# Kernel tuning notes

Hardware: AMD Instinct MI355X
Metric: run time of the kernel (lower is better)

Reference implementation:

```python
import jax, jax.numpy as jnp
import numpy as np

N = 100000
E = 2000000
F = 64          # in_features == out_features (required by attention * h_j)
BETA = 0.5
NEG_SLOPE = 0.01  # torch F.leaky_relu default


def setup_inputs() -> dict:
    key = jax.random.key(0)
    k1, k2, k3, k4, k5, k6 = jax.random.split(key, 6)
    h = jax.random.normal(k1, (N, F), dtype=jnp.float32)
    adj = jax.random.randint(k2, (2, E), 0, N, dtype=jnp.int64)
    amount = jax.random.uniform(k3, (E,), dtype=jnp.float32)
    count = jax.random.uniform(k4, (E,), dtype=jnp.float32)
    fc_w = jax.random.normal(k5, (F, 2 * F), dtype=jnp.float32) * (1.0 / np.sqrt(2 * F))
    fc_b = jax.random.normal(k6, (F,), dtype=jnp.float32) * 0.01
    return {"h": h, "adj": adj, "amount": amount, "count": count,
            "fc_w": fc_w, "fc_b": fc_b}


def _minmax_norm(x):
    lo, hi = x.min(), x.max()
    return (x - lo) / (hi - lo + 1e-8)


def reference(h, adj, amount, count, fc_w, fc_b):
    # per-edge weight from normalized amount/count
    edge_weight = BETA * _minmax_norm(amount) + (1.0 - BETA) * _minmax_norm(count)  # [E]

    src, dst = adj[0], adj[1]
    h_i = h[src]                     # [E, F]
    h_j = h[dst]                     # [E, F]
    h_cat = jnp.concatenate([h_i, h_j], axis=1)  # [E, 2F]

    score = jnp.einsum('ef,of->eo', h_cat, fc_w) + fc_b  # [E, F_out]
    score = jnp.where(score >= 0, score, NEG_SLOPE * score)  # leaky_relu
    score = score * edge_weight[:, None]

    # softmax over ALL edges (dim 0), per feature, as in the original
    attention = jax.nn.softmax(score, axis=0)  # [E, F]

    agg = jnp.zeros_like(h).at[src].add(attention * h_j)  # scatter-add -> [N, F]
    return agg
```

## Files before the change

kernel.cpp:

```cpp
#include <hip/hip_runtime.h>
#include <hip/hip_fp16.h>
#include <math.h>

#define FDIM   64
#define NB     16
#define MMB    512
#define BSHIFT 7
#define BMASK  127
#define EPTA   16
#define CHUNKA (EPTA * 256)
#define SCH    1024
#define DMASK  0xFFFFF

__global__ __launch_bounds__(256) void minmax1_k(const float* __restrict__ amount,
                                                 const float* __restrict__ count,
                                                 float4* __restrict__ partial,
                                                 double* __restrict__ colsum, int E4) {
  int idx = blockIdx.x * blockDim.x + threadIdx.x;
  int stride = gridDim.x * blockDim.x;
  if (idx < 64) colsum[idx] = 0.0;
  float amin = 3.4e38f, amax = -3.4e38f, cmin = 3.4e38f, cmax = -3.4e38f;
  const float4* a4 = (const float4*)amount;
  const float4* c4 = (const float4*)count;
  for (int i = idx; i < E4; i += stride) {
    float4 a = a4[i], c = c4[i];
    amin = fminf(amin, fminf(fminf(a.x, a.y), fminf(a.z, a.w)));
    amax = fmaxf(amax, fmaxf(fmaxf(a.x, a.y), fmaxf(a.z, a.w)));
    cmin = fminf(cmin, fminf(fminf(c.x, c.y), fminf(c.z, c.w)));
    cmax = fmaxf(cmax, fmaxf(fmaxf(c.x, c.y), fmaxf(c.z, c.w)));
  }
  #pragma unroll
  for (int off = 32; off; off >>= 1) {
    amin = fminf(amin, __shfl_down(amin, off));
    amax = fmaxf(amax, __shfl_down(amax, off));
    cmin = fminf(cmin, __shfl_down(cmin, off));
    cmax = fmaxf(cmax, __shfl_down(cmax, off));
  }
  __shared__ float4 lds[4];
  if ((threadIdx.x & 63) == 0) lds[threadIdx.x >> 6] = make_float4(amin, amax, cmin, cmax);
  __syncthreads();
  if (threadIdx.x == 0) {
    float4 r = lds[0];
    #pragma unroll
    for (int w = 1; w < 4; w++) {
      r.x = fminf(r.x, lds[w].x); r.y = fmaxf(r.y, lds[w].y);
      r.z = fminf(r.z, lds[w].z); r.w = fmaxf(r.w, lds[w].w);
    }
    partial[blockIdx.x] = r;
  }
}

__global__ __launch_bounds__(256) void minmax2_k(const float4* __restrict__ partial,
                                                 const float* __restrict__ amount,
                                                 const float* __restrict__ count,
                                                 float* __restrict__ mmf,
                                                 int nb, int E4, int E) {
  float amin = 3.4e38f, amax = -3.4e38f, cmin = 3.4e38f, cmax = -3.4e38f;
  for (int i = threadIdx.x; i < nb; i += 256) {
    float4 p = partial[i];
    amin = fminf(amin, p.x); amax = fmaxf(amax, p.y);
    cmin = fminf(cmin, p.z); cmax = fmaxf(cmax, p.w);
  }
  for (int i = 4 * E4 + threadIdx.x; i < E; i += 256) {
    float a = amount[i], c = count[i];
    amin = fminf(amin, a); amax = fmaxf(amax, a);
    cmin = fminf(cmin, c); cmax = fmaxf(cmax, c);
  }
  #pragma unroll
  for (int off = 32; off; off >>= 1) {
    amin = fminf(amin, __shfl_down(amin, off));
    amax = fmaxf(amax, __shfl_down(amax, off));
    cmin = fminf(cmin, __shfl_down(cmin, off));
    cmax = fmaxf(cmax, __shfl_down(cmax, off));
  }
  __shared__ float4 lds[4];
  if ((threadIdx.x & 63) == 0) lds[threadIdx.x >> 6] = make_float4(amin, amax, cmin, cmax);
  __syncthreads();
  if (threadIdx.x == 0) {
    float4 r = lds[0];
    #pragma unroll
    for (int w = 1; w < 4; w++) {
      r.x = fminf(r.x, lds[w].x); r.y = fmaxf(r.y, lds[w].y);
      r.z = fminf(r.z, lds[w].z); r.w = fmaxf(r.w, lds[w].w);
    }
    mmf[0] = r.x; mmf[1] = r.y; mmf[2] = r.z; mmf[3] = r.w;
  }
}

__global__ __launch_bounds__(256) void binA_count_k(const int* __restrict__ src,
                                                    int* __restrict__ mat,
                                                    int E, int nblkA, int nbkt) {
  __shared__ int lhist[1024];
  for (int k = threadIdx.x; k < nbkt; k += 256) lhist[k] = 0;
  __syncthreads();
  int e0 = blockIdx.x * CHUNKA + threadIdx.x * EPTA;
  if (e0 + EPTA <= E) {
    #pragma unroll
    for (int q = 0; q < EPTA; q += 4) {
      int4 s4 = *(const int4*)(src + e0 + q);
      atomicAdd(&lhist[s4.x >> BSHIFT], 1);
      atomicAdd(&lhist[s4.y >> BSHIFT], 1);
      atomicAdd(&lhist[s4.z >> BSHIFT], 1);
      atomicAdd(&lhist[s4.w >> BSHIFT], 1);
    }
  } else {
    for (int e = e0; e < E; e++) atomicAdd(&lhist[src[e] >> BSHIFT], 1);
  }
  __syncthreads();
  for (int k = threadIdx.x; k < nbkt; k += 256)
    mat[(size_t)k * nblkA + blockIdx.x] = lhist[k];
}

__global__ __launch_bounds__(256) void scan1_k(const int* __restrict__ v,
                                               int* __restrict__ bsum, int M) {
  __shared__ int lds[256];
  int t = threadIdx.x, b = blockIdx.x;
  int s = 0;
  for (int i = b * SCH + t; i < min((b + 1) * SCH, M); i += 256) s += v[i];
  lds[t] = s; __syncthreads();
  for (int off = 128; off; off >>= 1) {
    if (t < off) lds[t] += lds[t + off];
    __syncthreads();
  }
  if (t == 0) bsum[b] = lds[0];
}

__global__ __launch_bounds__(256) void scan2_k(const int* __restrict__ bsum,
                                               int* __restrict__ bexcl, int nchunk) {
  __shared__ int lds[256];
  int t = threadIdx.x;
  int running = 0;
  for (int c0 = 0; c0 < nchunk; c0 += 256) {
    int x = (c0 + t < nchunk) ? bsum[c0 + t] : 0;
    lds[t] = x; __syncthreads();
    for (int off = 1; off < 256; off <<= 1) {
      int v = (t >= off) ? lds[t - off] : 0;
      __syncthreads();
      lds[t] += v; __syncthreads();
    }
    if (c0 + t < nchunk) bexcl[c0 + t] = running + lds[t] - x;
    running += lds[255];
    __syncthreads();
  }
}

__global__ __launch_bounds__(256) void scan3_k(const int* __restrict__ v,
                                               const int* __restrict__ bexcl,
                                               int* __restrict__ smat, int M) {
  __shared__ int lds[256];
  int t = threadIdx.x, b = blockIdx.x;
  int running = bexcl[b];
  for (int tile = 0; tile < SCH; tile += 256) {
    int i = b * SCH + tile + t;
    int x = (i < M) ? v[i] : 0;
    lds[t] = x; __syncthreads();
    for (int off = 1; off < 256; off <<= 1) {
      int vv = (t >= off) ? lds[t - off] : 0;
      __syncthreads();
      lds[t] += vv; __syncthreads();
    }
    if (i < M) smat[i] = running + lds[t] - x;
    running += lds[255];
    __syncthreads();
  }
}

__global__ __launch_bounds__(256) void binA_scatter_k(const int* __restrict__ src,
                                                      const int* __restrict__ dst,
                                                      const float* __restrict__ amount,
                                                      const float* __restrict__ count,
                                                      const float* __restrict__ mmf,
                                                      const int* __restrict__ smat,
                                                      int2* __restrict__ payload,
                                                      int E, int nblkA, int nbkt) {
  __shared__ int lcur[1024];
  for (int k = threadIdx.x; k < nbkt; k += 256)
    lcur[k] = smat[(size_t)k * nblkA + blockIdx.x];
  __syncthreads();
  const float amin = mmf[0], amax = mmf[1], cmin = mmf[2], cmax = mmf[3];
  const float ascale = 0.5f / (amax - amin + 1e-8f);
  const float cscale = 0.5f / (cmax - cmin + 1e-8f);
  int e0 = blockIdx.x * CHUNKA + threadIdx.x * EPTA;
  if (e0 + EPTA <= E) {
    #pragma unroll
    for (int q = 0; q < EPTA; q += 4) {
      int4   s4 = *(const int4*)(src + e0 + q);
      int4   d4 = *(const int4*)(dst + e0 + q);
      float4 a4 = *(const float4*)(amount + e0 + q);
      float4 c4 = *(const float4*)(count + e0 + q);
      float w0 = (a4.x - amin) * ascale + (c4.x - cmin) * cscale;
      float w1 = (a4.y - amin) * ascale + (c4.y - cmin) * cscale;
      float w2 = (a4.z - amin) * ascale + (c4.z - cmin) * cscale;
      float w3 = (a4.w - amin) * ascale + (c4.w - cmin) * cscale;
      int p0 = atomicAdd(&lcur[s4.x >> BSHIFT], 1);
      int p1 = atomicAdd(&lcur[s4.y >> BSHIFT], 1);
      int p2 = atomicAdd(&lcur[s4.z >> BSHIFT], 1);
      int p3 = atomicAdd(&lcur[s4.w >> BSHIFT], 1);
      payload[p0] = make_int2(d4.x | ((s4.x & BMASK) << 20), __float_as_int(w0));
      payload[p1] = make_int2(d4.y | ((s4.y & BMASK) << 20), __float_as_int(w1));
      payload[p2] = make_int2(d4.z | ((s4.z & BMASK) << 20), __float_as_int(w2));
      payload[p3] = make_int2(d4.w | ((s4.w & BMASK) << 20), __float_as_int(w3));
    }
  } else {
    for (int e = e0; e < E; e++) {
      int s = src[e];
      float ew = (amount[e] - amin) * ascale + (count[e] - cmin) * cscale;
      int pos = atomicAdd(&lcur[s >> BSHIFT], 1);
      payload[pos] = make_int2(dst[e] | ((s & BMASK) << 20), __float_as_int(ew));
    }
  }
}

__global__ __launch_bounds__(256) void binB_k(const int2* __restrict__ payload,
                                              const int* __restrict__ smat,
                                              int* __restrict__ hist,
                                              int* __restrict__ offsets,
                                              int2* __restrict__ edge_s,
                                              int E, int nblkA, int nbkt, int N) {
  __shared__ int fcnt[128];
  __shared__ int fs[128];
  __shared__ int fcur[128];
  const int b = blockIdx.x;
  const int t = threadIdx.x;
  const int base = smat[(size_t)b * nblkA];
  const int end  = (b + 1 < nbkt) ? smat[(size_t)(b + 1) * nblkA] : E;
  if (t < 128) fcnt[t] = 0;
  __syncthreads();
  for (int i = base + t; i < end; i += 256)
    atomicAdd(&fcnt[payload[i].x >> 20], 1);
  __syncthreads();
  if (t < 128) fs[t] = fcnt[t];
  __syncthreads();
  for (int off = 1; off < 128; off <<= 1) {
    int v = 0;
    if (t < 128 && t >= off) v = fs[t - off];
    __syncthreads();
    if (t < 128) fs[t] += v;
    __syncthreads();
  }
  if (t < 128) {
    int excl = fs[t] - fcnt[t];
    fcur[t] = base + excl;
    int node = (b << BSHIFT) + t;
    if (node < N) { hist[node] = fcnt[t]; offsets[node] = base + excl; }
  }
  __syncthreads();
  for (int i = base + t; i < end; i += 256) {
    int2 v = payload[i];
    int pos = atomicAdd(&fcur[v.x >> 20], 1);
    edge_s[pos] = make_int2(v.x & DMASK, v.y);
  }
}

__global__ __launch_bounds__(128) void pre_gemm(const float* __restrict__ h,
                                                const float* __restrict__ fc_w,
                                                const float* __restrict__ fc_b,
                                                float* __restrict__ G1,
                                                __half2* __restrict__ P, int N) {
  __shared__ float hs[NB * FDIM];
  const int t = threadIdx.x;
  const int o = t & 63, half = t >> 6;
  float w[FDIM];
  const float* wrow = fc_w + o * 128 + half * 64;
  #pragma unroll
  for (int f = 0; f < FDIM; f += 4) {
    float4 v = *(const float4*)(wrow + f);
    w[f] = v.x; w[f + 1] = v.y; w[f + 2] = v.z; w[f + 3] = v.w;
  }
  const float bias = (half == 0) ? fc_b[o] : 0.0f;
  const int n0 = blockIdx.x * NB;
  const int nrows = min(NB, N - n0);
  for (int i = t; i < nrows * FDIM; i += 128) hs[i] = h[(size_t)n0 * FDIM + i];
  __syncthreads();
  for (int n = 0; n < nrows; n++) {
    float acc = bias;
    #pragma unroll
    for (int f = 0; f < FDIM; f += 4) {
      float4 hv = *(const float4*)(&hs[n * FDIM + f]);
      acc += hv.x * w[f] + hv.y * w[f + 1] + hv.z * w[f + 2] + hv.w * w[f + 3];
    }
    if (half == 0) {
      G1[(size_t)(n0 + n) * FDIM + o] = acc;
    } else {
      P[(size_t)(n0 + n) * FDIM + o] =
          __halves2half2(__float2half(acc), __float2half(hs[n * FDIM + o]));
    }
  }
}

__device__ __forceinline__ float2 unpack_h2(unsigned u) {
  __half2 v = *(__half2*)&u;
  return make_float2(__low2float(v), __high2float(v));
}

__global__ __launch_bounds__(256) void fused_k(const int* __restrict__ offsets,
                                               const int* __restrict__ hist,
                                               const int2* __restrict__ edge_s,
                                               const float* __restrict__ G1,
                                               const unsigned* __restrict__ P,
                                               double* __restrict__ colsum,
                                               float* __restrict__ out, int N) {
  const int lane = threadIdx.x & 63;
  const int wid = blockIdx.x * 4 + (threadIdx.x >> 6);
  const int nw = gridDim.x * 4;
  float csum = 0.0f;
  for (int n = wid; n < N; n += nw) {
    float g1 = G1[(size_t)n * FDIM + lane];
    float acc = 0.0f;
    int start = offsets[n], cnt = hist[n];
    for (int j0 = 0; j0 < cnt; j0 += 64) {
      int m = min(64, cnt - j0);
      int2 p = make_int2(0, 0);
      if (lane < m) p = edge_s[start + j0 + lane];
      int j = 0;
      for (; j + 8 <= m; j += 8) {
        int d0 = __builtin_amdgcn_readlane(p.x, j);
        int d1 = __builtin_amdgcn_readlane(p.x, j + 1);
        int d2 = __builtin_amdgcn_readlane(p.x, j + 2);
        int d3 = __builtin_amdgcn_readlane(p.x, j + 3);
        int d4 = __builtin_amdgcn_readlane(p.x, j + 4);
        int d5 = __builtin_amdgcn_readlane(p.x, j + 5);
        int d6 = __builtin_amdgcn_readlane(p.x, j + 6);
        int d7 = __builtin_amdgcn_readlane(p.x, j + 7);
        float e0 = __int_as_float(__builtin_amdgcn_readlane(p.y, j));
        float e1 = __int_as_float(__builtin_amdgcn_readlane(p.y, j + 1));
        float e2 = __int_as_float(__builtin_amdgcn_readlane(p.y, j + 2));
        float e3 = __int_as_float(__builtin_amdgcn_readlane(p.y, j + 3));
        float e4 = __int_as_float(__builtin_amdgcn_readlane(p.y, j + 4));
        float e5 = __int_as_float(__builtin_amdgcn_readlane(p.y, j + 5));
        float e6 = __int_as_float(__builtin_amdgcn_readlane(p.y, j + 6));
        float e7 = __int_as_float(__builtin_amdgcn_readlane(p.y, j + 7));
        unsigned u0 = P[(size_t)d0 * FDIM + lane];
        unsigned u1 = P[(size_t)d1 * FDIM + lane];
        unsigned u2 = P[(size_t)d2 * FDIM + lane];
        unsigned u3 = P[(size_t)d3 * FDIM + lane];
        unsigned u4 = P[(size_t)d4 * FDIM + lane];
        unsigned u5 = P[(size_t)d5 * FDIM + lane];
        unsigned u6 = P[(size_t)d6 * FDIM + lane];
        unsigned u7 = P[(size_t)d7 * FDIM + lane];
        float2 v0 = unpack_h2(u0), v1 = unpack_h2(u1), v2 = unpack_h2(u2), v3 = unpack_h2(u3);
        float2 v4 = unpack_h2(u4), v5 = unpack_h2(u5), v6 = unpack_h2(u6), v7 = unpack_h2(u7);
        float s0 = g1 + v0.x, s1 = g1 + v1.x, s2 = g1 + v2.x, s3 = g1 + v3.x;
        float s4 = g1 + v4.x, s5 = g1 + v5.x, s6 = g1 + v6.x, s7 = g1 + v7.x;
        s0 = (s0 >= 0.0f) ? s0 : 0.01f * s0;  s1 = (s1 >= 0.0f) ? s1 : 0.01f * s1;
        s2 = (s2 >= 0.0f) ? s2 : 0.01f * s2;  s3 = (s3 >= 0.0f) ? s3 : 0.01f * s3;
        s4 = (s4 >= 0.0f) ? s4 : 0.01f * s4;  s5 = (s5 >= 0.0f) ? s5 : 0.01f * s5;
        s6 = (s6 >= 0.0f) ? s6 : 0.01f * s6;  s7 = (s7 >= 0.0f) ? s7 : 0.01f * s7;
        float x0 = __expf(s0 * e0), x1 = __expf(s1 * e1);
        float x2 = __expf(s2 * e2), x3 = __expf(s3 * e3);
        float x4 = __expf(s4 * e4), x5 = __expf(s5 * e5);
        float x6 = __expf(s6 * e6), x7 = __expf(s7 * e7);
        csum += ((x0 + x1) + (x2 + x3)) + ((x4 + x5) + (x6 + x7));
        acc += x0 * v0.y + x1 * v1.y + x2 * v2.y + x3 * v3.y;
        acc += x4 * v4.y + x5 * v5.y + x6 * v6.y + x7 * v7.y;
      }
      for (; j < m; j++) {
        int d = __builtin_amdgcn_readlane(p.x, j);
        float ew = __int_as_float(__builtin_amdgcn_readlane(p.y, j));
        float2 v = unpack_h2(P[(size_t)d * FDIM + lane]);
        float sc = g1 + v.x;
        sc = (sc >= 0.0f) ? sc : 0.01f * sc;
        float x = __expf(sc * ew);
        csum += x;
        acc += x * v.y;
      }
    }
    out[(size_t)n * FDIM + lane] = acc;
  }
  __shared__ float part[256];
  part[threadIdx.x] = csum;
  __syncthreads();
  if (threadIdx.x < 64) {
    float tot = part[threadIdx.x] + part[threadIdx.x + 64] +
                part[threadIdx.x + 128] + part[threadIdx.x + 192];
    atomicAdd(&colsum[threadIdx.x], (double)tot);
  }
}

__global__ __launch_bounds__(256) void scale_k(float* __restrict__ out,
                                               const double* __restrict__ colsum,
                                               size_t total) {
  __shared__ float rinv_s[64];
  if (threadIdx.x < 64) rinv_s[threadIdx.x] = (float)(1.0 / colsum[threadIdx.x]);
  __syncthreads();
  const float r = rinv_s[threadIdx.x & 63];
  size_t idx = (size_t)blockIdx.x * blockDim.x + threadIdx.x;
  size_t stride = (size_t)gridDim.x * blockDim.x;
  for (size_t i = idx; i < total; i += stride) out[i] *= r;
}

extern "C" void kernel_launch(void* const* d_in, const int* in_sizes, int n_in,
                              void* d_out, int out_size, void* d_ws, size_t ws_size,
                              hipStream_t stream) {
  const float* h      = (const float*)d_in[0];
  const int*   adj    = (const int*)d_in[1];
  const float* amount = (const float*)d_in[2];
  const float* count  = (const float*)d_in[3];
  const float* fc_w   = (const float*)d_in[4];
  const float* fc_b   = (const float*)d_in[5];
  float* out = (float*)d_out;

  const int E = in_sizes[2];
  const int N = in_sizes[0] / FDIM;
  const int E4 = E / 4;
  const int* src = adj;
  const int* dst = adj + E;
  const int nbkt  = (N + BMASK) >> BSHIFT;
  const int nblkA = (E + CHUNKA - 1) / CHUNKA;
  const int M = nbkt * nblkA;
  const int nchunk = (M + SCH - 1) / SCH;

  char* ws = (char*)d_ws;
  size_t off = 0;
  auto alloc = [&](size_t bytes) { void* p = ws + off; off += (bytes + 255) & ~(size_t)255; return p; };
  float*    G1      = (float*)alloc((size_t)N * FDIM * sizeof(float));
  __half2*  P       = (__half2*)alloc((size_t)N * FDIM * sizeof(__half2));
  int2*     edge_s  = (int2*)alloc((size_t)E * sizeof(int2));
  int2*     payload = (int2*)alloc((size_t)E * sizeof(int2));
  int*      hist    = (int*)alloc((size_t)N * sizeof(int));
  int*      offsets = (int*)alloc((size_t)N * sizeof(int));
  int*      mat     = (int*)alloc((size_t)M * sizeof(int));
  int*      smat    = (int*)alloc((size_t)M * sizeof(int));
  int*      bsum    = (int*)alloc((size_t)nchunk * sizeof(int));
  int*      bexcl   = (int*)alloc((size_t)nchunk * sizeof(int));
  float4*   mmpart  = (float4*)alloc((size_t)MMB * sizeof(float4));
  double*   colsum  = (double*)alloc(64 * sizeof(double));
  float*    mmf     = (float*)alloc(4 * sizeof(float));

  minmax1_k<<<MMB, 256, 0, stream>>>(amount, count, mmpart, colsum, E4);
  minmax2_k<<<1, 256, 0, stream>>>(mmpart, amount, count, mmf, MMB, E4, E);
  binA_count_k<<<nblkA, 256, 0, stream>>>(src, mat, E, nblkA, nbkt);
  scan1_k<<<nchunk, 256, 0, stream>>>(mat, bsum, M);
  scan2_k<<<1, 256, 0, stream>>>(bsum, bexcl, nchunk);
  scan3_k<<<nchunk, 256, 0, stream>>>(mat, bexcl, smat, M);
  binA_scatter_k<<<nblkA, 256, 0, stream>>>(src, dst, amount, count, mmf, smat, payload, E, nblkA, nbkt);
  binB_k<<<nbkt, 256, 0, stream>>>(payload, smat, hist, offsets, edge_s, E, nblkA, nbkt, N);
  pre_gemm<<<(N + NB - 1) / NB, 128, 0, stream>>>(h, fc_w, fc_b, G1, P, N);
  fused_k<<<4096, 256, 0, stream>>>(offsets, hist, edge_s, G1, (const unsigned*)P, colsum, out, N);
  scale_k<<<2048, 256, 0, stream>>>(out, colsum, (size_t)N * FDIM);
}
```

Before: 338.2 us.

## Fuse minmax with bin counting, stage scatter in LDS, prefetch next node

Merges the amount/count min-max reduction into the bucket-count pass, so those arrays are read once and one launch disappears. The bucket scatter now sorts each block's edges locally in LDS before writing them to global memory, which makes the payload writes more contiguous. The aggregation loop prefetches the next node's offsets, G1 row and first edge batch, and replaces the remainder loop with masked groups of 8. The scale kernel is vectorised to float4. These add LDS pressure (about 50KB per scatter block, which may lower occupancy) and some extra wasted work in the masked tails.

Result: faster. 325.6 us (-3.7%).

```diff
diff --git a/kernel.cpp b/kernel.cpp
--- a/kernel.cpp
+++ b/kernel.cpp
@@ -4,7 +4,6 @@
 
 #define FDIM   64
 #define NB     16
-#define MMB    512
 #define BSHIFT 7
 #define BMASK  127
 #define EPTA   16
@@ -12,22 +11,42 @@
 #define SCH    1024
 #define DMASK  0xFFFFF
 
-__global__ __launch_bounds__(256) void minmax1_k(const float* __restrict__ amount,
-                                                 const float* __restrict__ count,
-                                                 float4* __restrict__ partial,
-                                                 double* __restrict__ colsum, int E4) {
-  int idx = blockIdx.x * blockDim.x + threadIdx.x;
-  int stride = gridDim.x * blockDim.x;
-  if (idx < 64) colsum[idx] = 0.0;
+__global__ __launch_bounds__(256) void count_mm_k(const int* __restrict__ src,
+                                                  const float* __restrict__ amount,
+                                                  const float* __restrict__ count,
+                                                  int* __restrict__ mat,
+                                                  float4* __restrict__ partial,
+                                                  double* __restrict__ colsum,
+                                                  int E, int nblkA, int nbkt) {
+  __shared__ int lhist[1024];
+  __shared__ float4 lred[4];
+  for (int k = threadIdx.x; k < nbkt; k += 256) lhist[k] = 0;
+  if (blockIdx.x == 0 && threadIdx.x < 64) colsum[threadIdx.x] = 0.0;
+  __syncthreads();
   float amin = 3.4e38f, amax = -3.4e38f, cmin = 3.4e38f, cmax = -3.4e38f;
-  const float4* a4 = (const float4*)amount;
-  const float4* c4 = (const float4*)count;
-  for (int i = idx; i < E4; i += stride) {
-    float4 a = a4[i], c = c4[i];
-    amin = fminf(amin, fminf(fminf(a.x, a.y), fminf(a.z, a.w)));
-    amax = fmaxf(amax, fmaxf(fmaxf(a.x, a.y), fmaxf(a.z, a.w)));
-    cmin = fminf(cmin, fminf(fminf(c.x, c.y), fminf(c.z, c.w)));
-    cmax = fmaxf(cmax, fmaxf(fmaxf(c.x, c.y), fmaxf(c.z, c.w)));
+  int e0 = blockIdx.x * CHUNKA + threadIdx.x * EPTA;
+  if (e0 + EPTA <= E) {
+    #pragma unroll
+    for (int q = 0; q < EPTA; q += 4) {
+      int4   s4 = *(const int4*)(src + e0 + q);
+      float4 a4 = *(const float4*)(amount + e0 + q);
+      float4 c4 = *(const float4*)(count + e0 + q);
+      atomicAdd(&lhist[s4.x >> BSHIFT], 1);
+      atomicAdd(&lhist[s4.y >> BSHIFT], 1);
+      atomicAdd(&lhist[s4.z >> BSHIFT], 1);
+      atomicAdd(&lhist[s4.w >> BSHIFT], 1);
+      amin = fminf(amin, fminf(fminf(a4.x, a4.y), fminf(a4.z, a4.w)));
+      amax = fmaxf(amax, fmaxf(fmaxf(a4.x, a4.y), fmaxf(a4.z, a4.w)));
+      cmin = fminf(cmin, fminf(fminf(c4.x, c4.y), fminf(c4.z, c4.w)));
+      cmax = fmaxf(cmax, fmaxf(fmaxf(c4.x, c4.y), fmaxf(c4.z, c4.w)));
+    }
+  } else {
+    for (int e = e0; e < E; e++) {
+      atomicAdd(&lhist[src[e] >> BSHIFT], 1);
+      float a = amount[e], c = count[e];
+      amin = fminf(amin, a); amax = fmaxf(amax, a);
+      cmin = fminf(cmin, c); cmax = fmaxf(cmax, c);
+    }
   }
   #pragma unroll
   for (int off = 32; off; off >>= 1) {
@@ -36,35 +55,28 @@
     cmin = fminf(cmin, __shfl_down(cmin, off));
     cmax = fmaxf(cmax, __shfl_down(cmax, off));
   }
-  __shared__ float4 lds[4];
-  if ((threadIdx.x & 63) == 0) lds[threadIdx.x >> 6] = make_float4(amin, amax, cmin, cmax);
-  __syncthreads();
+  if ((threadIdx.x & 63) == 0) lred[threadIdx.x >> 6] = make_float4(amin, amax, cmin, cmax);
+  __syncthreads();
+  for (int k = threadIdx.x; k < nbkt; k += 256)
+    mat[(size_t)k * nblkA + blockIdx.x] = lhist[k];
   if (threadIdx.x == 0) {
-    float4 r = lds[0];
+    float4 r = lred[0];
     #pragma unroll
     for (int w = 1; w < 4; w++) {
-      r.x = fminf(r.x, lds[w].x); r.y = fmaxf(r.y, lds[w].y);
-      r.z = fminf(r.z, lds[w].z); r.w = fmaxf(r.w, lds[w].w);
+      r.x = fminf(r.x, lred[w].x); r.y = fmaxf(r.y, lred[w].y);
+      r.z = fminf(r.z, lred[w].z); r.w = fmaxf(r.w, lred[w].w);
     }
     partial[blockIdx.x] = r;
   }
 }
 
 __global__ __launch_bounds__(256) void minmax2_k(const float4* __restrict__ partial,
-                                                 const float* __restrict__ amount,
-                                                 const float* __restrict__ count,
-                                                 float* __restrict__ mmf,
-                                                 int nb, int E4, int E) {
+                                                 float* __restrict__ mmf, int nb) {
   float amin = 3.4e38f, amax = -3.4e38f, cmin = 3.4e38f, cmax = -3.4e38f;
   for (int i = threadIdx.x; i < nb; i += 256) {
     float4 p = partial[i];
     amin = fminf(amin, p.x); amax = fmaxf(amax, p.y);
     cmin = fminf(cmin, p.z); cmax = fmaxf(cmax, p.w);
-  }
-  for (int i = 4 * E4 + threadIdx.x; i < E; i += 256) {
-    float a = amount[i], c = count[i];
-    amin = fminf(amin, a); amax = fmaxf(amax, a);
-    cmin = fminf(cmin, c); cmax = fmaxf(cmax, c);
   }
   #pragma unroll
   for (int off = 32; off; off >>= 1) {
@@ -85,30 +97,6 @@
     }
     mmf[0] = r.x; mmf[1] = r.y; mmf[2] = r.z; mmf[3] = r.w;
   }
-}
-
-__global__ __launch_bounds__(256) void binA_count_k(const int* __restrict__ src,
-                                                    int* __restrict__ mat,
-                                                    int E, int nblkA, int nbkt) {
-  __shared__ int lhist[1024];
-  for (int k = threadIdx.x; k < nbkt; k += 256) lhist[k] = 0;
-  __syncthreads();
-  int e0 = blockIdx.x * CHUNKA + threadIdx.x * EPTA;
-  if (e0 + EPTA <= E) {
-    #pragma unroll
-    for (int q = 0; q < EPTA; q += 4) {
-      int4 s4 = *(const int4*)(src + e0 + q);
-      atomicAdd(&lhist[s4.x >> BSHIFT], 1);
-      atomicAdd(&lhist[s4.y >> BSHIFT], 1);
-      atomicAdd(&lhist[s4.z >> BSHIFT], 1);
-      atomicAdd(&lhist[s4.w >> BSHIFT], 1);
-    }
-  } else {
-    for (int e = e0; e < E; e++) atomicAdd(&lhist[src[e] >> BSHIFT], 1);
-  }
-  __syncthreads();
-  for (int k = threadIdx.x; k < nbkt; k += 256)
-    mat[(size_t)k * nblkA + blockIdx.x] = lhist[k];
 }
 
 __global__ __launch_bounds__(256) void scan1_k(const int* __restrict__ v,
@@ -165,50 +153,84 @@
   }
 }
 
-__global__ __launch_bounds__(256) void binA_scatter_k(const int* __restrict__ src,
-                                                      const int* __restrict__ dst,
-                                                      const float* __restrict__ amount,
-                                                      const float* __restrict__ count,
-                                                      const float* __restrict__ mmf,
-                                                      const int* __restrict__ smat,
-                                                      int2* __restrict__ payload,
-                                                      int E, int nblkA, int nbkt) {
-  __shared__ int lcur[1024];
-  for (int k = threadIdx.x; k < nbkt; k += 256)
-    lcur[k] = smat[(size_t)k * nblkA + blockIdx.x];
+__global__ __launch_bounds__(256) void scatter_k(const int* __restrict__ src,
+                                                 const int* __restrict__ dst,
+                                                 const float* __restrict__ amount,
+                                                 const float* __restrict__ count,
+                                                 const float* __restrict__ mmf,
+                                                 const int* __restrict__ smat,
+                                                 int2* __restrict__ payload,
+                                                 int E, int nblkA, int nbkt) {
+  __shared__ int cntb[1024];
+  __shared__ int baseb[1024];
+  __shared__ int sbase[1024];
+  __shared__ int tmp[256];
+  __shared__ int2 lpay[CHUNKA];
+  __shared__ int lgpos[CHUNKA];
+  const int t = threadIdx.x, blk = blockIdx.x;
+  for (int k = t; k < nbkt; k += 256) {
+    cntb[k] = 0;
+    sbase[k] = smat[(size_t)k * nblkA + blk];
+  }
   __syncthreads();
   const float amin = mmf[0], amax = mmf[1], cmin = mmf[2], cmax = mmf[3];
   const float ascale = 0.5f / (amax - amin + 1e-8f);
   const float cscale = 0.5f / (cmax - cmin + 1e-8f);
-  int e0 = blockIdx.x * CHUNKA + threadIdx.x * EPTA;
-  if (e0 + EPTA <= E) {
-    #pragma unroll
-    for (int q = 0; q < EPTA; q += 4) {
-      int4   s4 = *(const int4*)(src + e0 + q);
-      int4   d4 = *(const int4*)(dst + e0 + q);
-      float4 a4 = *(const float4*)(amount + e0 + q);
-      float4 c4 = *(const float4*)(count + e0 + q);
-      float w0 = (a4.x - amin) * ascale + (c4.x - cmin) * cscale;
-      float w1 = (a4.y - amin) * ascale + (c4.y - cmin) * cscale;
-      float w2 = (a4.z - amin) * ascale + (c4.z - cmin) * cscale;
-      float w3 = (a4.w - amin) * ascale + (c4.w - cmin) * cscale;
-      int p0 = atomicAdd(&lcur[s4.x >> BSHIFT], 1);
-      int p1 = atomicAdd(&lcur[s4.y >> BSHIFT], 1);
-      int p2 = atomicAdd(&lcur[s4.z >> BSHIFT], 1);
-      int p3 = atomicAdd(&lcur[s4.w >> BSHIFT], 1);
-      payload[p0] = make_int2(d4.x | ((s4.x & BMASK) << 20), __float_as_int(w0));
-      payload[p1] = make_int2(d4.y | ((s4.y & BMASK) << 20), __float_as_int(w1));
-      payload[p2] = make_int2(d4.z | ((s4.z & BMASK) << 20), __float_as_int(w2));
-      payload[p3] = make_int2(d4.w | ((s4.w & BMASK) << 20), __float_as_int(w3));
+  int e0 = blk * CHUNKA + t * EPTA;
+  const bool full = (e0 + EPTA <= E);
+  int4   S[4]; int4 D[4]; float4 A[4]; float4 C[4];
+  if (full) {
+    #pragma unroll
+    for (int q = 0; q < 4; q++) {
+      S[q] = *(const int4*)(src + e0 + 4 * q);
+      D[q] = *(const int4*)(dst + e0 + 4 * q);
+      A[q] = *(const float4*)(amount + e0 + 4 * q);
+      C[q] = *(const float4*)(count + e0 + 4 * q);
+      atomicAdd(&cntb[S[q].x >> BSHIFT], 1);
+      atomicAdd(&cntb[S[q].y >> BSHIFT], 1);
+      atomicAdd(&cntb[S[q].z >> BSHIFT], 1);
+      atomicAdd(&cntb[S[q].w >> BSHIFT], 1);
     }
   } else {
-    for (int e = e0; e < E; e++) {
-      int s = src[e];
-      float ew = (amount[e] - amin) * ascale + (count[e] - cmin) * cscale;
-      int pos = atomicAdd(&lcur[s >> BSHIFT], 1);
-      payload[pos] = make_int2(dst[e] | ((s & BMASK) << 20), __float_as_int(ew));
-    }
-  }
+    for (int e = e0; e < E; e++) atomicAdd(&cntb[src[e] >> BSHIFT], 1);
+  }
+  __syncthreads();
+  int running = 0;
+  for (int c0 = 0; c0 < nbkt; c0 += 256) {
+    int x = (c0 + t < nbkt) ? cntb[c0 + t] : 0;
+    tmp[t] = x; __syncthreads();
+    for (int off = 1; off < 256; off <<= 1) {
+      int v = (t >= off) ? tmp[t - off] : 0;
+      __syncthreads();
+      tmp[t] += v; __syncthreads();
+    }
+    if (c0 + t < nbkt) baseb[c0 + t] = running + tmp[t] - x;
+    running += tmp[255];
+    __syncthreads();
+  }
+  for (int k = t; k < nbkt; k += 256) cntb[k] = baseb[k];
+  __syncthreads();
+  auto ins = [&](int s, int d, float a, float c) {
+    int b = s >> BSHIFT;
+    float ew = (a - amin) * ascale + (c - cmin) * cscale;
+    int pos = atomicAdd(&cntb[b], 1);
+    lpay[pos] = make_int2(d | ((s & BMASK) << 20), __float_as_int(ew));
+    lgpos[pos] = sbase[b] + (pos - baseb[b]);
+  };
+  if (full) {
+    #pragma unroll
+    for (int q = 0; q < 4; q++) {
+      ins(S[q].x, D[q].x, A[q].x, C[q].x);
+      ins(S[q].y, D[q].y, A[q].y, C[q].y);
+      ins(S[q].z, D[q].z, A[q].z, C[q].z);
+      ins(S[q].w, D[q].w, A[q].w, C[q].w);
+    }
+  } else {
+    for (int e = e0; e < E; e++) ins(src[e], dst[e], amount[e], count[e]);
+  }
+  __syncthreads();
+  const int ned = min(CHUNKA, E - blk * CHUNKA);
+  for (int i = t; i < ned; i += 256) payload[lgpos[i]] = lpay[i];
 }
 
 __global__ __launch_bounds__(256) void binB_k(const int2* __restrict__ payload,
@@ -304,68 +326,54 @@
   const int wid = blockIdx.x * 4 + (threadIdx.x >> 6);
   const int nw = gridDim.x * 4;
   float csum = 0.0f;
-  for (int n = wid; n < N; n += nw) {
-    float g1 = G1[(size_t)n * FDIM + lane];
+  int n = wid;
+  int start = 0, cnt = 0;
+  int2 p0 = make_int2(0, 0);
+  float g1 = 0.0f;
+  if (n < N) {
+    start = offsets[n]; cnt = hist[n];
+    g1 = G1[(size_t)n * FDIM + lane];
+    if (lane < cnt) p0 = edge_s[start + lane];
+  }
+  while (n < N) {
+    int nn = n + nw;
+    int startN = 0, cntN = 0; float g1N = 0.0f;
+    if (nn < N) {
+      startN = offsets[nn]; cntN = hist[nn];
+      g1N = G1[(size_t)nn * FDIM + lane];
+    }
     float acc = 0.0f;
-    int start = offsets[n], cnt = hist[n];
     for (int j0 = 0; j0 < cnt; j0 += 64) {
       int m = min(64, cnt - j0);
-      int2 p = make_int2(0, 0);
-      if (lane < m) p = edge_s[start + j0 + lane];
-      int j = 0;
-      for (; j + 8 <= m; j += 8) {
-        int d0 = __builtin_amdgcn_readlane(p.x, j);
-        int d1 = __builtin_amdgcn_readlane(p.x, j + 1);
-        int d2 = __builtin_amdgcn_readlane(p.x, j + 2);
-        int d3 = __builtin_amdgcn_readlane(p.x, j + 3);
-        int d4 = __builtin_amdgcn_readlane(p.x, j + 4);
-        int d5 = __builtin_amdgcn_readlane(p.x, j + 5);
-        int d6 = __builtin_amdgcn_readlane(p.x, j + 6);
-        int d7 = __builtin_amdgcn_readlane(p.x, j + 7);
-        float e0 = __int_as_float(__builtin_amdgcn_readlane(p.y, j));
-        float e1 = __int_as_float(__builtin_amdgcn_readlane(p.y, j + 1));
-        float e2 = __int_as_float(__builtin_amdgcn_readlane(p.y, j + 2));
-        float e3 = __int_as_float(__builtin_amdgcn_readlane(p.y, j + 3));
-        float e4 = __int_as_float(__builtin_amdgcn_readlane(p.y, j + 4));
-        float e5 = __int_as_float(__builtin_amdgcn_readlane(p.y, j + 5));
-        float e6 = __int_as_float(__builtin_amdgcn_readlane(p.y, j + 6));
-        float e7 = __int_as_float(__builtin_amdgcn_readlane(p.y, j + 7));
-        unsigned u0 = P[(size_t)d0 * FDIM + lane];
-        unsigned u1 = P[(size_t)d1 * FDIM + lane];
-        unsigned u2 = P[(size_t)d2 * FDIM + lane];
-        unsigned u3 = P[(size_t)d3 * FDIM + lane];
-        unsigned u4 = P[(size_t)d4 * FDIM + lane];
-        unsigned u5 = P[(size_t)d5 * FDIM + lane];
-        unsigned u6 = P[(size_t)d6 * FDIM + lane];
-        unsigned u7 = P[(size_t)d7 * FDIM + lane];
-        float2 v0 = unpack_h2(u0), v1 = unpack_h2(u1), v2 = unpack_h2(u2), v3 = unpack_h2(u3);
-        float2 v4 = unpack_h2(u4), v5 = unpack_h2(u5), v6 = unpack_h2(u6), v7 = unpack_h2(u7);
-        float s0 = g1 + v0.x, s1 = g1 + v1.x, s2 = g1 + v2.x, s3 = g1 + v3.x;
-        float s4 = g1 + v4.x, s5 = g1 + v5.x, s6 = g1 + v6.x, s7 = g1 + v7.x;
-        s0 = (s0 >= 0.0f) ? s0 : 0.01f * s0;  s1 = (s1 >= 0.0f) ? s1 : 0.01f * s1;
-        s2 = (s2 >= 0.0f) ? s2 : 0.01f * s2;  s3 = (s3 >= 0.0f) ? s3 : 0.01f * s3;
-        s4 = (s4 >= 0.0f) ? s4 : 0.01f * s4;  s5 = (s5 >= 0.0f) ? s5 : 0.01f * s5;
-        s6 = (s6 >= 0.0f) ? s6 : 0.01f * s6;  s7 = (s7 >= 0.0f) ? s7 : 0.01f * s7;
-        float x0 = __expf(s0 * e0), x1 = __expf(s1 * e1);
-        float x2 = __expf(s2 * e2), x3 = __expf(s3 * e3);
-        float x4 = __expf(s4 * e4), x5 = __expf(s5 * e5);
-        float x6 = __expf(s6 * e6), x7 = __expf(s7 * e7);
-        csum += ((x0 + x1) + (x2 + x3)) + ((x4 + x5) + (x6 + x7));
-        acc += x0 * v0.y + x1 * v1.y + x2 * v2.y + x3 * v3.y;
-        acc += x4 * v4.y + x5 * v5.y + x6 * v6.y + x7 * v7.y;
+      int2 p;
+      if (j0 == 0) p = p0;
+      else { p = make_int2(0, 0); if (lane < m) p = edge_s[start + j0 + lane]; }
+      for (int j = 0; j < m; j += 8) {
+        int rem = m - j;
+        int dd[8]; float ee[8], wm[8]; unsigned uu[8];
+        #pragma unroll
+        for (int k = 0; k < 8; k++) {
+          dd[k] = __builtin_amdgcn_readlane(p.x, j + k);
+          ee[k] = __int_as_float(__builtin_amdgcn_readlane(p.y, j + k));
+          wm[k] = (k < rem) ? 1.0f : 0.0f;
+        }
+        #pragma unroll
+        for (int k = 0; k < 8; k++) uu[k] = P[(size_t)dd[k] * FDIM + lane];
+        #pragma unroll
+        for (int k = 0; k < 8; k++) {
+          float2 v = unpack_h2(uu[k]);
+          float sc = g1 + v.x;
+          sc = (sc >= 0.0f) ? sc : 0.01f * sc;
+          float x = __expf(sc * ee[k]) * wm[k];
+          csum += x;
+          acc += x * v.y;
+        }
       }
-      for (; j < m; j++) {
-        int d = __builtin_amdgcn_readlane(p.x, j);
-        float ew = __int_as_float(__builtin_amdgcn_readlane(p.y, j));
-        float2 v = unpack_h2(P[(size_t)d * FDIM + lane]);
-        float sc = g1 + v.x;
-        sc = (sc >= 0.0f) ? sc : 0.01f * sc;
-        float x = __expf(sc * ew);
-        csum += x;
-        acc += x * v.y;
-      }
     }
     out[(size_t)n * FDIM + lane] = acc;
+    n = nn; start = startN; cnt = cntN; g1 = g1N;
+    p0 = make_int2(0, 0);
+    if (n < N && lane < min(cnt, 64)) p0 = edge_s[start + lane];
   }
   __shared__ float part[256];
   part[threadIdx.x] = csum;
@@ -377,16 +385,21 @@
   }
 }
 
-__global__ __launch_bounds__(256) void scale_k(float* __restrict__ out,
+__global__ __launch_bounds__(256) void scale_k(float4* __restrict__ out4,
                                                const double* __restrict__ colsum,
-                                               size_t total) {
+                                               int total4) {
   __shared__ float rinv_s[64];
   if (threadIdx.x < 64) rinv_s[threadIdx.x] = (float)(1.0 / colsum[threadIdx.x]);
   __syncthreads();
-  const float r = rinv_s[threadIdx.x & 63];
-  size_t idx = (size_t)blockIdx.x * blockDim.x + threadIdx.x;
-  size_t stride = (size_t)gridDim.x * blockDim.x;
-  for (size_t i = idx; i < total; i += stride) out[i] *= r;
+  const float4* r4 = (const float4*)rinv_s;
+  int idx = blockIdx.x * blockDim.x + threadIdx.x;
+  int stride = gridDim.x * blockDim.x;
+  for (int i = idx; i < total4; i += stride) {
+    float4 v = out4[i];
+    float4 r = r4[i & 15];
+    v.x *= r.x; v.y *= r.y; v.z *= r.z; v.w *= r.w;
+    out4[i] = v;
+  }
 }
 
 extern "C" void kernel_launch(void* const* d_in, const int* in_sizes, int n_in,
@@ -402,7 +415,6 @@
 
   const int E = in_sizes[2];
   const int N = in_sizes[0] / FDIM;
-  const int E4 = E / 4;
   const int* src = adj;
   const int* dst = adj + E;
   const int nbkt  = (N + BMASK) >> BSHIFT;
@@ -423,19 +435,18 @@
   int*      smat    = (int*)alloc((size_t)M * sizeof(int));
   int*      bsum    = (int*)alloc((size_t)nchunk * sizeof(int));
   int*      bexcl   = (int*)alloc((size_t)nchunk * sizeof(int));
-  float4*   mmpart  = (float4*)alloc((size_t)MMB * sizeof(float4));
+  float4*   mmpart  = (float4*)alloc((size_t)nblkA * sizeof(float4));
   double*   colsum  = (double*)alloc(64 * sizeof(double));
   float*    mmf     = (float*)alloc(4 * sizeof(float));
 
-  minmax1_k<<<MMB, 256, 0, stream>>>(amount, count, mmpart, colsum, E4);
-  minmax2_k<<<1, 256, 0, stream>>>(mmpart, amount, count, mmf, MMB, E4, E);
-  binA_count_k<<<nblkA, 256, 0, stream>>>(src, mat, E, nblkA, nbkt);
+  count_mm_k<<<nblkA, 256, 0, stream>>>(src, amount, count, mat, mmpart, colsum, E, nblkA, nbkt);
+  minmax2_k<<<1, 256, 0, stream>>>(mmpart, mmf, nblkA);
   scan1_k<<<nchunk, 256, 0, stream>>>(mat, bsum, M);
   scan2_k<<<1, 256, 0, stream>>>(bsum, bexcl, nchunk);
   scan3_k<<<nchunk, 256, 0, stream>>>(mat, bexcl, smat, M);
-  binA_scatter_k<<<nblkA, 256, 0, stream>>>(src, dst, amount, count, mmf, smat, payload, E, nblkA, nbkt);
+  scatter_k<<<nblkA, 256, 0, stream>>>(src, dst, amount, count, mmf, smat, payload, E, nblkA, nbkt);
   binB_k<<<nbkt, 256, 0, stream>>>(payload, smat, hist, offsets, edge_s, E, nblkA, nbkt, N);
   pre_gemm<<<(N + NB - 1) / NB, 128, 0, stream>>>(h, fc_w, fc_b, G1, P, N);
   fused_k<<<4096, 256, 0, stream>>>(offsets, hist, edge_s, G1, (const unsigned*)P, colsum, out, N);
-  scale_k<<<2048, 256, 0, stream>>>(out, colsum, (size_t)N * FDIM);
-}
+  scale_k<<<1024, 256, 0, stream>>>((float4*)out, colsum, N * FDIM / 4);
+}
```
